# Optimization experiments

Hardware: AMD Instinct MI355X
Metric: run time of the kernel (lower is better)

## Reference

```python
import jax, jax.numpy as jnp
import numpy as np

N_T = 80000      # tokens in document
N_S = 160000     # candidate spans (widths 1..2 -> ~2 per token)
D_STATE = 400    # states feature dim
D_EMB = 350      # embeds feature dim (hardcoded 350 in original)
D_DIST = 20      # distance embedding dim
H = 150          # Score hidden dim
W_MAX = 2        # max span width (L=2 in compute_idx_spans)
GI_DIM = 2 * D_STATE + D_EMB + D_DIST  # 1170
BINS = np.array([1, 2, 3, 4, 8, 16, 32, 64])


def _mlp(x, W1, b1, W2, b2, W3, b3):
    # Score module: Linear -> ReLU -> Linear -> ReLU -> Linear (dropout = identity at eval)
    h = jax.nn.relu(x @ W1 + b1)
    h = jax.nn.relu(h @ W2 + b2)
    return h @ W3 + b3


def setup_inputs() -> dict:
    key = jax.random.key(0)
    ks = jax.random.split(key, 18)

    def lin(k, fi, fo):
        return (jax.random.normal(k, (fi, fo), jnp.float32) / np.sqrt(fi)).astype(jnp.float32)

    states = jax.random.normal(ks[0], (N_T, D_STATE), jnp.float32)
    embeds = jax.random.normal(ks[1], (N_T, D_EMB), jnp.float32)
    span_starts = jnp.sort(jax.random.randint(ks[2], (N_S,), 0, N_T - 1))
    span_widths = jax.random.randint(ks[3], (N_S,), 0, W_MAX)  # i2 - i1 in {0,1}

    return {
        "states": states,
        "embeds": embeds,
        "span_starts": span_starts,
        "span_widths": span_widths,
        # attention Score params (attn_dim = D_STATE)
        "aW1": lin(ks[4], D_STATE, H), "ab1": jnp.zeros((H,), jnp.float32),
        "aW2": lin(ks[5], H, H),       "ab2": jnp.zeros((H,), jnp.float32),
        "aW3": lin(ks[6], H, 1),       "ab3": jnp.zeros((1,), jnp.float32),
        # width (Distance) embedding table: len(bins)+1 = 9 rows
        "width_table": 0.1 * jax.random.normal(ks[7], (len(BINS) + 1, D_DIST), jnp.float32),
        # mention Score params (gi_dim)
        "sW1": lin(ks[8], GI_DIM, H), "sb1": jnp.zeros((H,), jnp.float32),
        "sW2": lin(ks[9], H, H),      "sb2": jnp.zeros((H,), jnp.float32),
        "sW3": lin(ks[10], H, 1),     "sb3": jnp.zeros((1,), jnp.float32),
    }


def reference(states, embeds, span_starts, span_widths,
              aW1, ab1, aW2, ab2, aW3, ab3,
              width_table, sW1, sb1, sW2, sb2, sW3, sb3):
    n_t = states.shape[0]

    # alfa_t = attention(states): [n_t]
    alfa = _mlp(states, aW1, ab1, aW2, ab2, aW3, ab3)[:, 0]

    # Per-span softmax over the span's tokens (original: exp(alfa)/sum(exp(alfa[i1:i2+1])))
    offs = jnp.arange(W_MAX)                                  # [W]
    idx = span_starts[:, None] + offs[None, :]                # [n_s, W]
    mask = (offs[None, :] <= span_widths[:, None]).astype(alfa.dtype)
    idx_c = jnp.clip(idx, 0, n_t - 1)

    e = jnp.exp(alfa[idx_c]) * mask                           # [n_s, W]
    w = e / jnp.sum(e, axis=1, keepdims=True)                 # span-softmax weights

    # attn_embeds[i] = sum_j w_ij * embeds[i1+j]  -> [n_s, D_EMB]
    attn_embeds = jnp.einsum('sw,swd->sd', w, embeds[idx_c])

    # start/end state features
    span_ends = span_starts + span_widths
    start_end = jnp.concatenate([states[span_starts], states[span_ends]], axis=1)

    # width bin embedding: stoi(len) = #bins <= len
    lengths = span_widths + 1
    bin_idx = jnp.sum(lengths[:, None] >= jnp.asarray(BINS)[None, :], axis=1)
    width_emb = width_table[bin_idx]

    g_i = jnp.concatenate([start_end, attn_embeds, width_emb], axis=1)  # [n_s, GI_DIM]
    mention_scores = _mlp(g_i, sW1, sb1, sW2, sb2, sW3, sb3)            # [n_s, 1]
    return g_i, mention_scores
```

## Files before the change

kernel.cpp:

```cpp
#include <hip/hip_runtime.h>
#include <math.h>

#define N_T 80000
#define N_S 160000
#define D_STATE 400
#define D_EMB 350
#define D_DIST 20
#define HDIM 150
#define GI_DIM 1170
#define KP16 1216

typedef __attribute__((ext_vector_type(8))) short s16x8;
typedef __attribute__((ext_vector_type(4))) float f32x4;
typedef __attribute__((ext_vector_type(2))) float f32x2;

__device__ __forceinline__ unsigned short f2bf(float f) {
    union { float f; unsigned int u; } c; c.f = f;
    unsigned int u = c.u;
    unsigned int r = (u + 0x7fffu + ((u >> 16) & 1u)) >> 16;
    return (unsigned short)r;
}
__device__ __forceinline__ float bf2f(unsigned short h) {
    union { unsigned int u; float f; } c; c.u = ((unsigned int)h) << 16;
    return c.f;
}

__global__ __launch_bounds__(256) void convert_kernel(
    const float* __restrict__ sW1, const float* __restrict__ sW2, const float* __restrict__ sW3,
    const float* __restrict__ aW1, const float* __restrict__ aW2, const float* __restrict__ aW3,
    unsigned short* __restrict__ w1t_m, unsigned short* __restrict__ w2t_m, unsigned short* __restrict__ w3_m,
    unsigned short* __restrict__ w1t_a, unsigned short* __restrict__ w2t_a, unsigned short* __restrict__ w3_a)
{
    int gid = blockIdx.x * 256 + threadIdx.x;
    const int S1 = 160 * 1216, S2 = 160 * 160, S3 = 160, S4 = 160 * 448, S5 = 160 * 160, S6 = 160;
    if (gid < S1) {
        int n = gid / 1216, k = gid % 1216;
        float v = (k < GI_DIM && n < HDIM) ? sW1[k * HDIM + n] : 0.f;
        w1t_m[gid] = f2bf(v); return;
    } gid -= S1;
    if (gid < S2) {
        int n = gid / 160, k = gid % 160;
        float v = (k < HDIM && n < HDIM) ? sW2[k * HDIM + n] : 0.f;
        w2t_m[gid] = f2bf(v); return;
    } gid -= S2;
    if (gid < S3) { w3_m[gid] = (gid < HDIM) ? f2bf(sW3[gid]) : (unsigned short)0; return; } gid -= S3;
    if (gid < S4) {
        int n = gid / 448, k = gid % 448;
        float v = (k < D_STATE && n < HDIM) ? aW1[k * HDIM + n] : 0.f;
        w1t_a[gid] = f2bf(v); return;
    } gid -= S4;
    if (gid < S5) {
        int n = gid / 160, k = gid % 160;
        float v = (k < HDIM && n < HDIM) ? aW2[k * HDIM + n] : 0.f;
        w2t_a[gid] = f2bf(v); return;
    } gid -= S5;
    if (gid < S6) { w3_a[gid] = (gid < HDIM) ? f2bf(aW3[gid]) : (unsigned short)0; }
}

template <int W16>
__global__ __launch_bounds__(256) void gi_build(
    const float* __restrict__ states, const float* __restrict__ embeds,
    const int* __restrict__ starts, const int* __restrict__ widths,
    const float* __restrict__ alfa, const float* __restrict__ wtab,
    float* __restrict__ gi, unsigned short* __restrict__ gi16)
{
    const int wave = threadIdx.x >> 6;
    const int lane = threadIdx.x & 63;
    const int s = blockIdx.x * 4 + wave;

    const int i1 = starts[s];
    const int wdt = widths[s];
    int i2 = i1 + wdt; if (i2 > N_T - 1) i2 = N_T - 1;
    int ie = i1 + 1;  if (ie > N_T - 1) ie = N_T - 1;

    const float e0 = expf(alfa[i1]);
    const float e1 = (wdt > 0) ? expf(alfa[ie]) : 0.0f;
    const float inv = 1.0f / (e0 + e1);
    const float w0 = e0 * inv;
    const float w1v = e1 * inv;

    const float* __restrict__ sp1 = states + (size_t)i1 * D_STATE;
    const float* __restrict__ sp2 = states + (size_t)i2 * D_STATE;
    const float* __restrict__ em1 = embeds + (size_t)i1 * D_EMB;
    const float* __restrict__ em2 = embeds + (size_t)ie * D_EMB;
    const float* __restrict__ wt = wtab + (size_t)(wdt + 1) * D_DIST;
    float* __restrict__ grow = gi + (size_t)s * GI_DIM;
    unsigned short* __restrict__ hrow = W16 ? (gi16 + (size_t)s * KP16) : (unsigned short*)0;

    float v[5][4];
#pragma unroll
    for (int i = 0; i < 5; ++i) {
        const int j = (i * 64 + lane) * 4;
        if (j + 4 <= 400) {
            float4 q = *(const float4*)(sp1 + j);
            v[i][0] = q.x; v[i][1] = q.y; v[i][2] = q.z; v[i][3] = q.w;
        } else if (j >= 400 && j + 4 <= 800) {
            float4 q = *(const float4*)(sp2 + (j - 400));
            v[i][0] = q.x; v[i][1] = q.y; v[i][2] = q.z; v[i][3] = q.w;
        } else if (j >= 800 && j + 4 <= 1148) {
            const int jj = j - 800;
            float2 a0 = *(const float2*)(em1 + jj);
            float2 a1 = *(const float2*)(em1 + jj + 2);
            float2 b0 = *(const float2*)(em2 + jj);
            float2 b1 = *(const float2*)(em2 + jj + 2);
            v[i][0] = w0 * a0.x + w1v * b0.x;
            v[i][1] = w0 * a0.y + w1v * b0.y;
            v[i][2] = w0 * a1.x + w1v * b1.x;
            v[i][3] = w0 * a1.y + w1v * b1.y;
        } else if (j < KP16) {
#pragma unroll
            for (int q = 0; q < 4; ++q) {
                const int jq = j + q;
                float val;
                if (jq < 400) val = sp1[jq];
                else if (jq < 800) val = sp2[jq - 400];
                else if (jq < 1150) val = w0 * em1[jq - 800] + w1v * em2[jq - 800];
                else if (jq < GI_DIM) val = wt[jq - 1150];
                else val = 0.f;
                v[i][q] = val;
            }
        }
    }

#pragma unroll
    for (int i = 0; i < 5; ++i) {
        const int j = (i * 64 + lane) * 4;
        if (j >= KP16) continue;
        if (W16) {
            uint2 p;
            p.x = (unsigned int)f2bf(v[i][0]) | ((unsigned int)f2bf(v[i][1]) << 16);
            p.y = (unsigned int)f2bf(v[i][2]) | ((unsigned int)f2bf(v[i][3]) << 16);
            *(uint2*)(hrow + j) = p;
        }
        if (j + 2 <= GI_DIM) {
            f32x2 p01; p01.x = v[i][0]; p01.y = v[i][1];
            __builtin_nontemporal_store(p01, (f32x2*)(grow + j));
        }
        if (j + 4 <= GI_DIM) {
            f32x2 p23; p23.x = v[i][2]; p23.y = v[i][3];
            __builtin_nontemporal_store(p23, (f32x2*)(grow + j + 2));
        }
    }
}

__global__ __launch_bounds__(256) void mention_gemm(
    const unsigned short* __restrict__ A16,
    const unsigned short* __restrict__ w1t, const float* __restrict__ b1,
    const unsigned short* __restrict__ w2t, const float* __restrict__ b2,
    const unsigned short* __restrict__ w3, const float* __restrict__ b3,
    float* __restrict__ out)
{
    __shared__ __align__(16) char smem[43008];
    const int SB_OFF = 16384;

    const int tid = threadIdx.x;
    const int w = tid >> 6;
    const int l = tid & 63;
    const int l15 = l & 15;
    const int lg = l >> 4;
    const int row0 = blockIdx.x * 128;

    f32x4 acc[2][10];
#pragma unroll
    for (int rf = 0; rf < 2; ++rf)
#pragma unroll
        for (int nf = 0; nf < 10; ++nf) acc[rf][nf] = (f32x4){0.f, 0.f, 0.f, 0.f};

    const int arow_base = w * 32 + l15;
    const int asw = (arow_base & 7) << 4;

    s16x8 va[4], vb[5];
    {
        const int k0 = 0;
#pragma unroll
        for (int i = 0; i < 4; ++i) {
            int j = i * 256 + tid; int row = j >> 3, sub = j & 7;
            va[i] = *(const s16x8*)(A16 + (size_t)(row0 + row) * KP16 + k0 + sub * 8);
        }
#pragma unroll
        for (int i = 0; i < 5; ++i) {
            int idx = i * 256 + tid; int n = idx >> 3, s2 = idx & 7;
            vb[i] = *(const s16x8*)(w1t + (size_t)n * KP16 + k0 + s2 * 8);
        }
    }

    for (int t = 0; t < 19; ++t) {
        __syncthreads();

#pragma unroll
        for (int i = 0; i < 4; ++i) {
            int j = i * 256 + tid; int row = j >> 3, sub = j & 7;
            *(s16x8*)(smem + row * 128 + ((sub * 16) ^ ((row & 7) << 4))) = va[i];
        }
#pragma unroll
        for (int i = 0; i < 5; ++i) {
            int idx = i * 256 + tid; int n = idx >> 3, s2 = idx & 7;
            *(s16x8*)(smem + SB_OFF + n * 128 + ((s2 * 16) ^ ((n & 7) << 4))) = vb[i];
        }
        __syncthreads();

        if (t + 1 < 19) {
            const int k0 = (t + 1) * 64;
#pragma unroll
            for (int i = 0; i < 4; ++i) {
                int j = i * 256 + tid; int row = j >> 3, sub = j & 7;
                va[i] = *(const s16x8*)(A16 + (size_t)(row0 + row) * KP16 + k0 + sub * 8);
            }
#pragma unroll
            for (int i = 0; i < 5; ++i) {
                int idx = i * 256 + tid; int n = idx >> 3, s2 = idx & 7;
                vb[i] = *(const s16x8*)(w1t + (size_t)n * KP16 + k0 + s2 * 8);
            }
        }

#pragma unroll
        for (int kc = 0; kc < 2; ++kc) {
            const int inrowA = kc * 64 + lg * 16;
            s16x8 a0 = *(const s16x8*)(smem + arow_base * 128 + (inrowA ^ asw));
            s16x8 a1 = *(const s16x8*)(smem + arow_base * 128 + 2048 + (inrowA ^ asw));
#pragma unroll
            for (int nf = 0; nf < 10; ++nf) {
                const int n = nf * 16 + l15;
                s16x8 b = *(const s16x8*)(smem + SB_OFF + n * 128 + (inrowA ^ ((n & 7) << 4)));
                acc[0][nf] = __builtin_amdgcn_mfma_f32_16x16x32_bf16(a0, b, acc[0][nf], 0, 0, 0);
                acc[1][nf] = __builtin_amdgcn_mfma_f32_16x16x32_bf16(a1, b, acc[1][nf], 0, 0, 0);
            }
        }
    }

    __syncthreads();

    {
        float b1c[10];
#pragma unroll
        for (int nf = 0; nf < 10; ++nf) {
            int col = nf * 16 + l15;
            b1c[nf] = (col < HDIM) ? b1[col] : 0.f;
        }
#pragma unroll
        for (int rf = 0; rf < 2; ++rf)
#pragma unroll
            for (int nf = 0; nf < 10; ++nf)
#pragma unroll
                for (int r = 0; r < 4; ++r) {
                    int row = w * 32 + rf * 16 + lg * 4 + r;
                    int col = nf * 16 + l15;
                    float h = fmaxf(acc[rf][nf][r] + b1c[nf], 0.f);
                    *(unsigned short*)(smem + row * 336 + col * 2) = f2bf(h);
                }
    }
    __syncthreads();

    f32x4 acc2[2][10];
#pragma unroll
    for (int rf = 0; rf < 2; ++rf)
#pragma unroll
        for (int nf = 0; nf < 10; ++nf) acc2[rf][nf] = (f32x4){0.f, 0.f, 0.f, 0.f};

#pragma unroll
    for (int kc = 0; kc < 5; ++kc) {
        s16x8 a0 = *(const s16x8*)(smem + (w * 32 + l15) * 336 + kc * 64 + lg * 16);
        s16x8 a1 = *(const s16x8*)(smem + (w * 32 + 16 + l15) * 336 + kc * 64 + lg * 16);
#pragma unroll
        for (int nf = 0; nf < 10; ++nf) {
            const int n = nf * 16 + l15;
            s16x8 b = *(const s16x8*)(w2t + n * 160 + kc * 32 + lg * 8);
            acc2[0][nf] = __builtin_amdgcn_mfma_f32_16x16x32_bf16(a0, b, acc2[0][nf], 0, 0, 0);
            acc2[1][nf] = __builtin_amdgcn_mfma_f32_16x16x32_bf16(a1, b, acc2[1][nf], 0, 0, 0);
        }
    }

    {
        float b2c[10], w3c[10];
#pragma unroll
        for (int nf = 0; nf < 10; ++nf) {
            int col = nf * 16 + l15;
            b2c[nf] = (col < HDIM) ? b2[col] : 0.f;
            w3c[nf] = bf2f(w3[col]);
        }
#pragma unroll
        for (int rf = 0; rf < 2; ++rf)
#pragma unroll
            for (int r = 0; r < 4; ++r) {
                float ps = 0.f;
#pragma unroll
                for (int nf = 0; nf < 10; ++nf)
                    ps += fmaxf(acc2[rf][nf][r] + b2c[nf], 0.f) * w3c[nf];
                ps += __shfl_xor(ps, 1);
                ps += __shfl_xor(ps, 2);
                ps += __shfl_xor(ps, 4);
                ps += __shfl_xor(ps, 8);
                if (l15 == 0)
                    out[row0 + w * 32 + rf * 16 + lg * 4 + r] = ps + b3[0];
            }
    }
}

template <int K, int NT>
__global__ __launch_bounds__(256) void mlp_mfma(
    const float* __restrict__ A,
    const unsigned short* __restrict__ w1t, const float* __restrict__ b1,
    const unsigned short* __restrict__ w2t, const float* __restrict__ b2,
    const unsigned short* __restrict__ w3, const float* __restrict__ b3,
    float* __restrict__ out)
{
    constexpr int KP = NT * 64;
    __shared__ __align__(16) char smem[43008];
    const int SB_OFF = 16384;

    const int tid = threadIdx.x;
    const int w = tid >> 6;
    const int l = tid & 63;
    const int l15 = l & 15;
    const int lg = l >> 4;
    const int row0 = blockIdx.x * 128;

    const int arow = tid >> 1;
    const int acb = (tid & 1) * 32;

    f32x4 acc[2][10];
#pragma unroll
    for (int rf = 0; rf < 2; ++rf)
#pragma unroll
        for (int nf = 0; nf < 10; ++nf) acc[rf][nf] = (f32x4){0.f, 0.f, 0.f, 0.f};

    const int arow_base = w * 32 + l15;
    const int asw = (arow_base & 7) << 4;

    for (int t = 0; t < NT; ++t) {
        const int k0 = t * 64;
        __syncthreads();

        unsigned short tmp[32];
        if (k0 + 64 <= K) {
            const float* src = A + (size_t)(row0 + arow) * K + k0 + acb;
#pragma unroll
            for (int i = 0; i < 16; ++i) {
                float2 v = ((const float2*)src)[i];
                tmp[2 * i] = f2bf(v.x);
                tmp[2 * i + 1] = f2bf(v.y);
            }
        } else {
            const float* arp = A + (size_t)(row0 + arow) * K;
#pragma unroll
            for (int i = 0; i < 32; ++i) {
                int col = k0 + acb + i;
                tmp[i] = (col < K) ? f2bf(arp[col]) : (unsigned short)0;
            }
        }
        {
            const int sw = (arow & 7) << 4;
#pragma unroll
            for (int i = 0; i < 4; ++i) {
                s16x8 pv;
#pragma unroll
                for (int j = 0; j < 8; ++j) pv[j] = (short)tmp[i * 8 + j];
                int inrow = acb * 2 + i * 16;
                *(s16x8*)(smem + arow * 128 + (inrow ^ sw)) = pv;
            }
        }

#pragma unroll
        for (int i = 0; i < 5; ++i) {
            int idx = i * 256 + tid;
            int n = idx >> 3, s2 = idx & 7;
            s16x8 v = *(const s16x8*)(w1t + (size_t)n * KP + k0 + s2 * 8);
            int inrow = s2 * 16;
            *(s16x8*)(smem + SB_OFF + n * 128 + (inrow ^ ((n & 7) << 4))) = v;
        }

        __syncthreads();

#pragma unroll
        for (int kc = 0; kc < 2; ++kc) {
            const int inrowA = kc * 64 + lg * 16;
            s16x8 a0 = *(const s16x8*)(smem + arow_base * 128 + (inrowA ^ asw));
            s16x8 a1 = *(const s16x8*)(smem + arow_base * 128 + 2048 + (inrowA ^ asw));
#pragma unroll
            for (int nf = 0; nf < 10; ++nf) {
                const int n = nf * 16 + l15;
                s16x8 b = *(const s16x8*)(smem + SB_OFF + n * 128 + (inrowA ^ ((n & 7) << 4)));
                acc[0][nf] = __builtin_amdgcn_mfma_f32_16x16x32_bf16(a0, b, acc[0][nf], 0, 0, 0);
                acc[1][nf] = __builtin_amdgcn_mfma_f32_16x16x32_bf16(a1, b, acc[1][nf], 0, 0, 0);
            }
        }
    }

    __syncthreads();

    {
        float b1c[10];
#pragma unroll
        for (int nf = 0; nf < 10; ++nf) {
            int col = nf * 16 + l15;
            b1c[nf] = (col < HDIM) ? b1[col] : 0.f;
        }
#pragma unroll
        for (int rf = 0; rf < 2; ++rf)
#pragma unroll
            for (int nf = 0; nf < 10; ++nf)
#pragma unroll
                for (int r = 0; r < 4; ++r) {
                    int row = w * 32 + rf * 16 + lg * 4 + r;
                    int col = nf * 16 + l15;
                    float h = fmaxf(acc[rf][nf][r] + b1c[nf], 0.f);
                    *(unsigned short*)(smem + row * 336 + col * 2) = f2bf(h);
                }
    }
    __syncthreads();

    f32x4 acc2[2][10];
#pragma unroll
    for (int rf = 0; rf < 2; ++rf)
#pragma unroll
        for (int nf = 0; nf < 10; ++nf) acc2[rf][nf] = (f32x4){0.f, 0.f, 0.f, 0.f};

#pragma unroll
    for (int kc = 0; kc < 5; ++kc) {
        s16x8 a0 = *(const s16x8*)(smem + (w * 32 + l15) * 336 + kc * 64 + lg * 16);
        s16x8 a1 = *(const s16x8*)(smem + (w * 32 + 16 + l15) * 336 + kc * 64 + lg * 16);
#pragma unroll
        for (int nf = 0; nf < 10; ++nf) {
            const int n = nf * 16 + l15;
            s16x8 b = *(const s16x8*)(w2t + n * 160 + kc * 32 + lg * 8);
            acc2[0][nf] = __builtin_amdgcn_mfma_f32_16x16x32_bf16(a0, b, acc2[0][nf], 0, 0, 0);
            acc2[1][nf] = __builtin_amdgcn_mfma_f32_16x16x32_bf16(a1, b, acc2[1][nf], 0, 0, 0);
        }
    }

    {
        float b2c[10], w3c[10];
#pragma unroll
        for (int nf = 0; nf < 10; ++nf) {
            int col = nf * 16 + l15;
            b2c[nf] = (col < HDIM) ? b2[col] : 0.f;
            w3c[nf] = bf2f(w3[col]);
        }
#pragma unroll
        for (int rf = 0; rf < 2; ++rf)
#pragma unroll
            for (int r = 0; r < 4; ++r) {
                float ps = 0.f;
#pragma unroll
                for (int nf = 0; nf < 10; ++nf)
                    ps += fmaxf(acc2[rf][nf][r] + b2c[nf], 0.f) * w3c[nf];
                ps += __shfl_xor(ps, 1);
                ps += __shfl_xor(ps, 2);
                ps += __shfl_xor(ps, 4);
                ps += __shfl_xor(ps, 8);
                if (l15 == 0)
                    out[row0 + w * 32 + rf * 16 + lg * 4 + r] = ps + b3[0];
            }
    }
}

extern "C" void kernel_launch(void* const* d_in, const int* in_sizes, int n_in,
                              void* d_out, int out_size, void* d_ws, size_t ws_size,
                              hipStream_t stream)
{
    const float* states = (const float*)d_in[0];
    const float* embeds = (const float*)d_in[1];
    const int*   starts = (const int*)d_in[2];
    const int*   widths = (const int*)d_in[3];
    const float* aW1 = (const float*)d_in[4];
    const float* ab1 = (const float*)d_in[5];
    const float* aW2 = (const float*)d_in[6];
    const float* ab2 = (const float*)d_in[7];
    const float* aW3 = (const float*)d_in[8];
    const float* ab3 = (const float*)d_in[9];
    const float* wtab = (const float*)d_in[10];
    const float* sW1 = (const float*)d_in[11];
    const float* sb1 = (const float*)d_in[12];
    const float* sW2 = (const float*)d_in[13];
    const float* sb2 = (const float*)d_in[14];
    const float* sW3 = (const float*)d_in[15];
    const float* sb3 = (const float*)d_in[16];

    float* gi = (float*)d_out;
    float* scores = gi + (size_t)N_S * GI_DIM;

    char* ws = (char*)d_ws;
    float* alfa = (float*)ws;
    unsigned short* w1t_m = (unsigned short*)(ws + 320512);
    unsigned short* w2t_m = (unsigned short*)(ws + 709632);
    unsigned short* w3_m  = (unsigned short*)(ws + 760832);
    unsigned short* w1t_a = (unsigned short*)(ws + 761344);
    unsigned short* w2t_a = (unsigned short*)(ws + 904704);
    unsigned short* w3_a  = (unsigned short*)(ws + 955904);
    const size_t GI16_OFF = 956416;
    const size_t GI16_BYTES = (size_t)N_S * KP16 * 2;
    unsigned short* gi16 = (unsigned short*)(ws + GI16_OFF);
    const bool have_ws = (ws_size >= GI16_OFF + GI16_BYTES);

    convert_kernel<<<1242, 256, 0, stream>>>(sW1, sW2, sW3, aW1, aW2, aW3,
                                             w1t_m, w2t_m, w3_m, w1t_a, w2t_a, w3_a);

    mlp_mfma<D_STATE, 7><<<N_T / 128, 256, 0, stream>>>(
        states, w1t_a, ab1, w2t_a, ab2, w3_a, ab3, alfa);

    if (have_ws) {
        gi_build<1><<<N_S / 4, 256, 0, stream>>>(
            states, embeds, starts, widths, alfa, wtab, gi, gi16);
        mention_gemm<<<N_S / 128, 256, 0, stream>>>(
            gi16, w1t_m, sb1, w2t_m, sb2, w3_m, sb3, scores);
    } else {
        gi_build<0><<<N_S / 4, 256, 0, stream>>>(
            states, embeds, starts, widths, alfa, wtab, gi, (unsigned short*)0);
        mlp_mfma<GI_DIM, 19><<<N_S / 128, 256, 0, stream>>>(
            gi, w1t_m, sb1, w2t_m, sb2, w3_m, sb3, scores);
    }
}
```

Before: 507.4 us.

## Double-buffer A tile in LDS and read W1 fragments directly from global

```diff
diff --git a/kernel.cpp b/kernel.cpp
--- a/kernel.cpp
+++ b/kernel.cpp
@@ -143,7 +143,7 @@
     }
 }
 
-__global__ __launch_bounds__(256) void mention_gemm(
+__global__ __launch_bounds__(256) void mention_gemm3(
     const unsigned short* __restrict__ A16,
     const unsigned short* __restrict__ w1t, const float* __restrict__ b1,
     const unsigned short* __restrict__ w2t, const float* __restrict__ b2,
@@ -151,7 +151,6 @@
     float* __restrict__ out)
 {
     __shared__ __align__(16) char smem[43008];
-    const int SB_OFF = 16384;
 
     const int tid = threadIdx.x;
     const int w = tid >> 6;
@@ -169,35 +168,21 @@
     const int arow_base = w * 32 + l15;
     const int asw = (arow_base & 7) << 4;
 
-    s16x8 va[4], vb[5];
-    {
-        const int k0 = 0;
-#pragma unroll
-        for (int i = 0; i < 4; ++i) {
-            int j = i * 256 + tid; int row = j >> 3, sub = j & 7;
-            va[i] = *(const s16x8*)(A16 + (size_t)(row0 + row) * KP16 + k0 + sub * 8);
-        }
-#pragma unroll
-        for (int i = 0; i < 5; ++i) {
-            int idx = i * 256 + tid; int n = idx >> 3, s2 = idx & 7;
-            vb[i] = *(const s16x8*)(w1t + (size_t)n * KP16 + k0 + s2 * 8);
-        }
-    }
+    s16x8 va[4];
+#pragma unroll
+    for (int i = 0; i < 4; ++i) {
+        int j = i * 256 + tid; int row = j >> 3, sub = j & 7;
+        va[i] = *(const s16x8*)(A16 + (size_t)(row0 + row) * KP16 + sub * 8);
+    }
+#pragma unroll
+    for (int i = 0; i < 4; ++i) {
+        int j = i * 256 + tid; int row = j >> 3, sub = j & 7;
+        *(s16x8*)(smem + row * 128 + ((sub * 16) ^ ((row & 7) << 4))) = va[i];
+    }
+    __syncthreads();
 
     for (int t = 0; t < 19; ++t) {
-        __syncthreads();
-
-#pragma unroll
-        for (int i = 0; i < 4; ++i) {
-            int j = i * 256 + tid; int row = j >> 3, sub = j & 7;
-            *(s16x8*)(smem + row * 128 + ((sub * 16) ^ ((row & 7) << 4))) = va[i];
-        }
-#pragma unroll
-        for (int i = 0; i < 5; ++i) {
-            int idx = i * 256 + tid; int n = idx >> 3, s2 = idx & 7;
-            *(s16x8*)(smem + SB_OFF + n * 128 + ((s2 * 16) ^ ((n & 7) << 4))) = vb[i];
-        }
-        __syncthreads();
+        const char* sA = smem + (t & 1) * 16384;
 
         if (t + 1 < 19) {
             const int k0 = (t + 1) * 64;
@@ -206,29 +191,34 @@
                 int j = i * 256 + tid; int row = j >> 3, sub = j & 7;
                 va[i] = *(const s16x8*)(A16 + (size_t)(row0 + row) * KP16 + k0 + sub * 8);
             }
-#pragma unroll
-            for (int i = 0; i < 5; ++i) {
-                int idx = i * 256 + tid; int n = idx >> 3, s2 = idx & 7;
-                vb[i] = *(const s16x8*)(w1t + (size_t)n * KP16 + k0 + s2 * 8);
-            }
-        }
-
+        }
+
+        const unsigned short* __restrict__ bk = w1t + t * 64;
 #pragma unroll
         for (int kc = 0; kc < 2; ++kc) {
             const int inrowA = kc * 64 + lg * 16;
-            s16x8 a0 = *(const s16x8*)(smem + arow_base * 128 + (inrowA ^ asw));
-            s16x8 a1 = *(const s16x8*)(smem + arow_base * 128 + 2048 + (inrowA ^ asw));
+            s16x8 a0 = *(const s16x8*)(sA + arow_base * 128 + (inrowA ^ asw));
+            s16x8 a1 = *(const s16x8*)(sA + arow_base * 128 + 2048 + (inrowA ^ asw));
+            const unsigned short* __restrict__ bkk = bk + kc * 32 + lg * 8;
 #pragma unroll
             for (int nf = 0; nf < 10; ++nf) {
                 const int n = nf * 16 + l15;
-                s16x8 b = *(const s16x8*)(smem + SB_OFF + n * 128 + (inrowA ^ ((n & 7) << 4)));
+                s16x8 b = *(const s16x8*)(bkk + (size_t)n * KP16);
                 acc[0][nf] = __builtin_amdgcn_mfma_f32_16x16x32_bf16(a0, b, acc[0][nf], 0, 0, 0);
                 acc[1][nf] = __builtin_amdgcn_mfma_f32_16x16x32_bf16(a1, b, acc[1][nf], 0, 0, 0);
             }
         }
-    }
-
-    __syncthreads();
+
+        if (t + 1 < 19) {
+            char* sAn = smem + ((t + 1) & 1) * 16384;
+#pragma unroll
+            for (int i = 0; i < 4; ++i) {
+                int j = i * 256 + tid; int row = j >> 3, sub = j & 7;
+                *(s16x8*)(sAn + row * 128 + ((sub * 16) ^ ((row & 7) << 4))) = va[i];
+            }
+        }
+        __syncthreads();
+    }
 
     {
         float b1c[10];
@@ -501,7 +491,7 @@
     if (have_ws) {
         gi_build<1><<<N_S / 4, 256, 0, stream>>>(
             states, embeds, starts, widths, alfa, wtab, gi, gi16);
-        mention_gemm<<<N_S / 128, 256, 0, stream>>>(
+        mention_gemm3<<<N_S / 128, 256, 0, stream>>>(
             gi16, w1t_m, sb1, w2t_m, sb2, w3_m, sb3, scores);
     } else {
         gi_build<0><<<N_S / 4, 256, 0, stream>>>(
```

Measured after the change: 758.7 us. +49.5%, slower.
